# Kernel optimization log

Hardware: AMD Instinct MI355X
Metric: run time of the kernel (lower is better)

Reference implementation:

```python
import jax, jax.numpy as jnp
import numpy as np

ZONEOUT = 0.15  # deterministic (eval-mode) zoneout on the output gate
HIDDEN = 128


def setup_inputs() -> dict:
    key = jax.random.key(0)
    k1, k2, k3, k4 = jax.random.split(key, 4)
    B, T, D, H = 512, 256, 256, HIDDEN
    x = jax.random.normal(k1, (B, T, D), dtype=jnp.float32)
    # gate projection for [i, f, o, g] gates, fan-in scaled
    Wx = jax.random.normal(k2, (4 * H, D), dtype=jnp.float32) / np.sqrt(D)
    Wh = jax.random.normal(k3, (4 * H, H), dtype=jnp.float32) / np.sqrt(H)
    b = jax.random.normal(k4, (4 * H,), dtype=jnp.float32) * 0.01
    return {"x": x, "Wx": Wx, "Wh": Wh, "b": b}


def reference(x, Wx, Wh, b):
    # x: [B, T, D]; returns (hids, cels, pogs) each [B, T, H]
    B, T, D = x.shape
    H = Wh.shape[1]
    z = jnp.asarray(ZONEOUT, dtype=x.dtype)

    def step(carry, xt):
        hid, cel, pog = carry  # each [B, H]
        gates = xt @ Wx.T + hid @ Wh.T + b  # [B, 4H]
        i_pre, f_pre, o_pre, g_pre = jnp.split(gates, 4, axis=-1)
        i = jax.nn.sigmoid(i_pre)
        f = jax.nn.sigmoid(f_pre)
        g = jnp.tanh(g_pre)
        # zoneout on the output gate: blend with previous output gate
        o = (1.0 - z) * jax.nn.sigmoid(o_pre) + z * pog
        cel_new = f * cel + i * g
        hid_new = o * jnp.tanh(cel_new)
        return (hid_new, cel_new, o), (hid_new, cel_new, o)

    zeros = jnp.zeros((B, H), dtype=x.dtype)
    xs = jnp.swapaxes(x, 0, 1)  # [T, B, D]
    _, (hids, cels, pogs) = jax.lax.scan(step, (zeros, zeros, zeros), xs)
    # [T, B, H] -> [B, T, H]
    return (jnp.swapaxes(hids, 0, 1), jnp.swapaxes(cels, 0, 1), jnp.swapaxes(pogs, 0, 1))
```

## Files before the change

### kernel.cpp

```cpp
#include <hip/hip_runtime.h>

typedef __attribute__((ext_vector_type(8))) short     bf16x8;
typedef __attribute__((ext_vector_type(4))) float     f32x4;
typedef __attribute__((ext_vector_type(4))) unsigned short ushort4_t;

#define BSZ   512
#define TSZ   256
#define DSZ   256
#define HSZ   128
#define G4    512
#define OUT1  16777216L

__device__ inline unsigned short f2bf(float f) {
  union { float f; unsigned int u; } v; v.f = f;
  unsigned int r = (v.u + 0x7FFFu + ((v.u >> 16) & 1u)) >> 16;
  return (unsigned short)r;
}
__device__ inline float bf2f(unsigned int s) {
  union { unsigned int u; float f; } v; v.u = s << 16;
  return v.f;
}
__device__ inline float sig_fast(float x)  { return 1.0f / (1.0f + __expf(-x)); }
__device__ inline float tanh_fast(float x) { return 1.0f - 2.0f / (__expf(2.0f * x) + 1.0f); }

__global__ __launch_bounds__(256)
void gemm_xw(const float* __restrict__ x, const float* __restrict__ Wx,
             const float* __restrict__ bias, unsigned short* __restrict__ xw) {
  __shared__ unsigned short aF[16384];
  __shared__ unsigned short bF[16384];

  const int tid   = threadIdx.x;
  const long mBase = (long)blockIdx.y * 64;
  const int  nBase = blockIdx.x * 64;

  const float* aSrc = x  + mBase * DSZ;
  const float* bSrc = Wx + (long)nBase * DSZ;

#pragma unroll
  for (int i = 0; i < 16; ++i) {
    int e  = i * 1024 + tid * 4;
    int m  = e >> 8, k = e & 255;
    int c  = k >> 5, kk = k & 31;
    int ln = (m & 15) | ((kk >> 3) << 4);
    int j  = kk & 7;
    int mt = m >> 4;
    int dst = (((c << 2) + mt) * 64 + ln) * 8 + j;
    float4 va = *(const float4*)(aSrc + e);
    float4 vb = *(const float4*)(bSrc + e);
    ushort4_t pa, pb;
    pa.x = f2bf(va.x); pa.y = f2bf(va.y); pa.z = f2bf(va.z); pa.w = f2bf(va.w);
    pb.x = f2bf(vb.x); pb.y = f2bf(vb.y); pb.z = f2bf(vb.z); pb.w = f2bf(vb.w);
    *(ushort4_t*)&aF[dst] = pa;
    *(ushort4_t*)&bF[dst] = pb;
  }
  __syncthreads();

  const int w = tid >> 6, lane = tid & 63;
  f32x4 acc[4];
#pragma unroll
  for (int nt = 0; nt < 4; ++nt) acc[nt] = (f32x4){0.f, 0.f, 0.f, 0.f};

#pragma unroll
  for (int c = 0; c < 8; ++c) {
    bf16x8 av = *(const bf16x8*)&aF[(((c << 2) + w) * 64 + lane) * 8];
#pragma unroll
    for (int nt = 0; nt < 4; ++nt) {
      bf16x8 bv = *(const bf16x8*)&bF[(((c << 2) + nt) * 64 + lane) * 8];
      acc[nt] = __builtin_amdgcn_mfma_f32_16x16x32_bf16(av, bv, acc[nt], 0, 0, 0);
    }
  }

  const int colLoc = lane & 15, rowQ = lane >> 4;
#pragma unroll
  for (int nt = 0; nt < 4; ++nt) {
    int n = nBase + nt * 16 + colLoc;
    float bv = bias[n];
#pragma unroll
    for (int r = 0; r < 4; ++r) {
      long m = mBase + w * 16 + rowQ * 4 + r;
      long row = (m & (TSZ - 1)) * BSZ + (m >> 8);
      xw[row * (long)G4 + n] = f2bf(acc[nt][r] + bv);
    }
  }
}

__global__ __launch_bounds__(512, 2)
void lstm_rec_mfma(const unsigned short* __restrict__ xw, const float* __restrict__ Wh,
                   float* __restrict__ outH, float* __restrict__ outC,
                   float* __restrict__ outP) {
  __shared__ unsigned short h_lds[2 * 2048];

  const int tid  = threadIdx.x;
  const int w    = tid >> 6;
  const int lane = tid & 63;
  const int p    = lane & 15;
  const int r16  = lane >> 4;
  const int b0   = blockIdx.x * 2;

  bf16x8 whF[4][4];
#pragma unroll
  for (int q = 0; q < 4; ++q) {
#pragma unroll
    for (int c = 0; c < 4; ++c) {
      const float* src = Wh + ((q * 128 + w * 16 + p) * HSZ + c * 32 + r16 * 8);
      float4 lo = *(const float4*)src;
      float4 hi = *(const float4*)(src + 4);
      bf16x8 f;
      f[0] = (short)f2bf(lo.x); f[1] = (short)f2bf(lo.y);
      f[2] = (short)f2bf(lo.z); f[3] = (short)f2bf(lo.w);
      f[4] = (short)f2bf(hi.x); f[5] = (short)f2bf(hi.y);
      f[6] = (short)f2bf(hi.z); f[7] = (short)f2bf(hi.w);
      whF[q][c] = f;
    }
  }

  for (int i = tid; i < 2 * 2048; i += 512) h_lds[i] = 0;

  float cel0 = 0.f, cel1 = 0.f, pog0 = 0.f, pog1 = 0.f;

  const int colw = w * 16 + p;
  const int c_  = colw >> 5, kk = colw & 31;
  const int lhi = (kk >> 3) << 4, jj = kk & 7;
  const int wr0 = c_ * 512 + (0 | lhi) * 8 + jj;
  const int wr1 = c_ * 512 + (1 | lhi) * 8 + jj;

  const unsigned short* xp = xw + (long)b0 * G4;
  const long XSTR = (long)BSZ * G4;

  unsigned int xvA[8], xvB[8];
#pragma unroll
  for (int q = 0; q < 4; ++q) {
    xvA[2 * q]     = xp[colw + q * 128];
    xvA[2 * q + 1] = xp[colw + G4 + q * 128];
  }
  xp += XSTR;

  float* pH0 = outH + (long)b0 * TSZ * HSZ;
  float* pC0 = outC + (long)b0 * TSZ * HSZ;
  float* pP0 = outP + (long)b0 * TSZ * HSZ;
  float* pH1 = pH0 + (long)TSZ * HSZ;
  float* pC1 = pC0 + (long)TSZ * HSZ;
  float* pP1 = pP0 + (long)TSZ * HSZ;

  f32x4 acc[4];
#pragma unroll
  for (int q = 0; q < 4; ++q) acc[q] = (f32x4){0.f, 0.f, 0.f, 0.f};

  __syncthreads();

#define STEP(RDOFF, WROFF, XC, XN, PREF)                                        \
  {                                                                             \
    bf16x8 aF[4];                                                               \
    _Pragma("unroll")                                                           \
    for (int c = 0; c < 4; ++c)                                                 \
      aF[c] = *(const bf16x8*)&h_lds[(RDOFF) + c * 512 + lane * 8];             \
    if (PREF) {                                                                 \
      _Pragma("unroll")                                                         \
      for (int q = 0; q < 4; ++q) {                                             \
        XN[2 * q]     = xp[colw + q * 128];                                     \
        XN[2 * q + 1] = xp[colw + G4 + q * 128];                                \
      }                                                                         \
      xp += XSTR;                                                               \
    }                                                                           \
    _Pragma("unroll")                                                           \
    for (int q = 0; q < 4; ++q) {                                               \
      acc[q][0] = bf2f(XC[2 * q]);                                              \
      acc[q][1] = bf2f(XC[2 * q + 1]);                                          \
    }                                                                           \
    _Pragma("unroll")                                                           \
    for (int q = 0; q < 4; ++q)                                                 \
      _Pragma("unroll")                                                         \
      for (int c = 0; c < 4; ++c)                                               \
        acc[q] = __builtin_amdgcn_mfma_f32_16x16x32_bf16(aF[c], whF[q][c], acc[q], 0, 0, 0); \
    float i0 = sig_fast(acc[0][0]), i1 = sig_fast(acc[0][1]);                   \
    float f0 = sig_fast(acc[1][0]), f1 = sig_fast(acc[1][1]);                   \
    float s0 = sig_fast(acc[2][0]), s1 = sig_fast(acc[2][1]);                   \
    float o0 = 0.85f * s0 + 0.15f * pog0, o1 = 0.85f * s1 + 0.15f * pog1;       \
    float g0 = tanh_fast(acc[3][0]), g1 = tanh_fast(acc[3][1]);                 \
    cel0 = f0 * cel0 + i0 * g0; cel1 = f1 * cel1 + i1 * g1;                     \
    float h0 = o0 * tanh_fast(cel0), h1 = o1 * tanh_fast(cel1);                 \
    pog0 = o0; pog1 = o1;                                                       \
    if (lane < 16) {                                                            \
      pH0[colw] = h0; pC0[colw] = cel0; pP0[colw] = o0;                         \
      pH1[colw] = h1; pC1[colw] = cel1; pP1[colw] = o1;                         \
      h_lds[(WROFF) + wr0] = f2bf(h0);                                          \
      h_lds[(WROFF) + wr1] = f2bf(h1);                                          \
    }                                                                           \
    pH0 += HSZ; pC0 += HSZ; pP0 += HSZ;                                         \
    pH1 += HSZ; pC1 += HSZ; pP1 += HSZ;                                         \
    asm volatile("s_waitcnt lgkmcnt(0)" ::: "memory");    \
    __builtin_amdgcn_s_barrier();                        \
  }

  for (int it = 0; it < 127; ++it) {
    STEP(0, 2048, xvA, xvB, true)
    STEP(2048, 0, xvB, xvA, true)
  }
  STEP(0, 2048, xvA, xvB, true)
  STEP(2048, 0, xvB, xvA, false)
#undef STEP
}

extern "C" void kernel_launch(void* const* d_in, const int* in_sizes, int n_in,
                              void* d_out, int out_size, void* d_ws, size_t ws_size,
                              hipStream_t stream) {
  const float* x    = (const float*)d_in[0];
  const float* Wx   = (const float*)d_in[1];
  const float* Wh   = (const float*)d_in[2];
  const float* bias = (const float*)d_in[3];

  float* outH = (float*)d_out;
  float* outC = outH + OUT1;
  float* outP = outC + OUT1;

  unsigned short* xwp = (unsigned short*)d_ws;

  dim3 g1(8, 2048), tb1(256);
  dim3 g2(256),     tb2(512);

  gemm_xw<<<g1, tb1, 0, stream>>>(x, Wx, bias, xwp);
  lstm_rec_mfma<<<g2, tb2, 0, stream>>>(xwp, Wh, outH, outC, outP);
}
```

Measured before the change: 703.2 us.

## Keep Wx fragments in registers and stream x tiles with double-buffered LDS

Rewrites the input-projection GEMM so each block of 512 threads converts and holds all Wx gate-column fragments in registers and loops over 32 tiles of 16 rows of x. The next tile's global load is prefetched into registers while the current tile's MFMAs run, using a two-slot LDS buffer. The bias is folded into the accumulator initialisation. This removes the repeated Wx loads and bf16 conversion done by every block of the old grid and cuts the block count, at the cost of heavy register use (32 bf16x8 fragments per thread) and narrow 2-byte stores.

```diff
diff --git a/kernel.cpp b/kernel.cpp
--- a/kernel.cpp
+++ b/kernel.cpp
@@ -2,7 +2,6 @@
 
 typedef __attribute__((ext_vector_type(8))) short     bf16x8;
 typedef __attribute__((ext_vector_type(4))) float     f32x4;
-typedef __attribute__((ext_vector_type(4))) unsigned short ushort4_t;
 
 #define BSZ   512
 #define TSZ   256
@@ -23,63 +22,83 @@
 __device__ inline float sig_fast(float x)  { return 1.0f / (1.0f + __expf(-x)); }
 __device__ inline float tanh_fast(float x) { return 1.0f - 2.0f / (__expf(2.0f * x) + 1.0f); }
 
-__global__ __launch_bounds__(256)
+__global__ __launch_bounds__(512, 2)
 void gemm_xw(const float* __restrict__ x, const float* __restrict__ Wx,
              const float* __restrict__ bias, unsigned short* __restrict__ xw) {
-  __shared__ unsigned short aF[16384];
-  __shared__ unsigned short bF[16384];
-
-  const int tid   = threadIdx.x;
-  const long mBase = (long)blockIdx.y * 64;
-  const int  nBase = blockIdx.x * 64;
-
-  const float* aSrc = x  + mBase * DSZ;
-  const float* bSrc = Wx + (long)nBase * DSZ;
-
-#pragma unroll
-  for (int i = 0; i < 16; ++i) {
-    int e  = i * 1024 + tid * 4;
-    int m  = e >> 8, k = e & 255;
-    int c  = k >> 5, kk = k & 31;
-    int ln = (m & 15) | ((kk >> 3) << 4);
-    int j  = kk & 7;
-    int mt = m >> 4;
-    int dst = (((c << 2) + mt) * 64 + ln) * 8 + j;
-    float4 va = *(const float4*)(aSrc + e);
-    float4 vb = *(const float4*)(bSrc + e);
-    ushort4_t pa, pb;
-    pa.x = f2bf(va.x); pa.y = f2bf(va.y); pa.z = f2bf(va.z); pa.w = f2bf(va.w);
-    pb.x = f2bf(vb.x); pb.y = f2bf(vb.y); pb.z = f2bf(vb.z); pb.w = f2bf(vb.w);
-    *(ushort4_t*)&aF[dst] = pa;
-    *(ushort4_t*)&bF[dst] = pb;
-  }
-  __syncthreads();
-
-  const int w = tid >> 6, lane = tid & 63;
-  f32x4 acc[4];
-#pragma unroll
-  for (int nt = 0; nt < 4; ++nt) acc[nt] = (f32x4){0.f, 0.f, 0.f, 0.f};
-
-#pragma unroll
-  for (int c = 0; c < 8; ++c) {
-    bf16x8 av = *(const bf16x8*)&aF[(((c << 2) + w) * 64 + lane) * 8];
-#pragma unroll
-    for (int nt = 0; nt < 4; ++nt) {
-      bf16x8 bv = *(const bf16x8*)&bF[(((c << 2) + nt) * 64 + lane) * 8];
-      acc[nt] = __builtin_amdgcn_mfma_f32_16x16x32_bf16(av, bv, acc[nt], 0, 0, 0);
-    }
-  }
-
-  const int colLoc = lane & 15, rowQ = lane >> 4;
+  __shared__ unsigned short aT[2][4096];
+
+  const int tid = threadIdx.x;
+  const int w   = tid >> 6;
+  const int l   = tid & 63;
+  const int p   = l & 15;
+  const int r16 = l >> 4;
+  const long m0blk = (long)blockIdx.x * 512;
+
+  bf16x8 wf[4][8];
 #pragma unroll
   for (int nt = 0; nt < 4; ++nt) {
-    int n = nBase + nt * 16 + colLoc;
-    float bv = bias[n];
+#pragma unroll
+    for (int c = 0; c < 8; ++c) {
+      const float* src = Wx + (long)(w * 64 + nt * 16 + p) * DSZ + c * 32 + r16 * 8;
+      float4 lo = *(const float4*)src;
+      float4 hi = *(const float4*)(src + 4);
+      bf16x8 f;
+      f[0] = (short)f2bf(lo.x); f[1] = (short)f2bf(lo.y);
+      f[2] = (short)f2bf(lo.z); f[3] = (short)f2bf(lo.w);
+      f[4] = (short)f2bf(hi.x); f[5] = (short)f2bf(hi.y);
+      f[6] = (short)f2bf(hi.z); f[7] = (short)f2bf(hi.w);
+      wf[nt][c] = f;
+    }
+  }
+  float bn[4];
+#pragma unroll
+  for (int nt = 0; nt < 4; ++nt) bn[nt] = bias[w * 64 + nt * 16 + p];
+
+  const float* asrc = x + (m0blk + (l & 15)) * DSZ + (4 * w + r16) * 8;
+  const int wl8 = (w * 64 + l) * 8;
+
+  float4 va = *(const float4*)asrc;
+  float4 vb = *(const float4*)(asrc + 4);
+  asrc += 16 * DSZ;
+
+  for (int i = 0; i < 32; ++i) {
+    bf16x8 fr;
+    fr[0] = (short)f2bf(va.x); fr[1] = (short)f2bf(va.y);
+    fr[2] = (short)f2bf(va.z); fr[3] = (short)f2bf(va.w);
+    fr[4] = (short)f2bf(vb.x); fr[5] = (short)f2bf(vb.y);
+    fr[6] = (short)f2bf(vb.z); fr[7] = (short)f2bf(vb.w);
+    *(bf16x8*)&aT[i & 1][wl8] = fr;
+
+    if (i < 31) {
+      va = *(const float4*)asrc;
+      vb = *(const float4*)(asrc + 4);
+      asrc += 16 * DSZ;
+    }
+
+    asm volatile("s_waitcnt lgkmcnt(0)" ::: "memory");
+    __builtin_amdgcn_s_barrier();
+
+    f32x4 acc[4];
+#pragma unroll
+    for (int nt = 0; nt < 4; ++nt)
+      acc[nt] = (f32x4){bn[nt], bn[nt], bn[nt], bn[nt]};
+
+#pragma unroll
+    for (int c = 0; c < 8; ++c) {
+      bf16x8 aF = *(const bf16x8*)&aT[i & 1][(c * 64 + l) * 8];
+#pragma unroll
+      for (int nt = 0; nt < 4; ++nt)
+        acc[nt] = __builtin_amdgcn_mfma_f32_16x16x32_bf16(aF, wf[nt][c], acc[nt], 0, 0, 0);
+    }
+
+    const long rowbase = ((long)((i & 15) * 16 + r16 * 4) * BSZ + (blockIdx.x * 2 + (i >> 4))) * G4
+                         + w * 64 + p;
 #pragma unroll
     for (int r = 0; r < 4; ++r) {
-      long m = mBase + w * 16 + rowQ * 4 + r;
-      long row = (m & (TSZ - 1)) * BSZ + (m >> 8);
-      xw[row * (long)G4 + n] = f2bf(acc[nt][r] + bv);
+      const long rb = rowbase + (long)r * (BSZ * G4);
+#pragma unroll
+      for (int nt = 0; nt < 4; ++nt)
+        xw[rb + nt * 16] = f2bf(acc[nt][r]);
     }
   }
 }
@@ -215,8 +234,8 @@
 
   unsigned short* xwp = (unsigned short*)d_ws;
 
-  dim3 g1(8, 2048), tb1(256);
-  dim3 g2(256),     tb2(512);
+  dim3 g1(256), tb1(512);
+  dim3 g2(256), tb2(512);
 
   gemm_xw<<<g1, tb1, 0, stream>>>(x, Wx, bias, xwp);
   lstm_rec_mfma<<<g2, tb2, 0, stream>>>(xwp, Wh, outH, outC, outP);
```

Result: faster. 585.8 us (-16.7%).
